# Kernel optimization log

Measured on AMD Instinct MI355X. Metric: run time of the kernel, lower is better.

## Reference

```python
import jax, jax.numpy as jnp
import numpy as np

N_NODES = 100000
IN_DIM = 128
HID = 128
N_REL = 2
N_EDGES = 500000


def setup_inputs() -> dict:
    key = jax.random.key(0)
    ks = jax.random.split(key, 12)
    x = jax.random.normal(ks[0], (N_NODES, IN_DIM), dtype=jnp.float32)
    edge_index = jax.random.randint(ks[1], (2, N_EDGES), 0, N_NODES, dtype=jnp.int64)
    edge_type = jax.random.randint(ks[2], (N_EDGES,), 0, N_REL, dtype=jnp.int64)
    def w(k, shape, fan_in):
        return jax.random.normal(k, shape, dtype=jnp.float32) / np.sqrt(fan_in)
    return {
        "x": x,
        "edge_index": edge_index,
        "edge_type": edge_type,
        "W_rel1": w(ks[3], (N_REL, IN_DIM, HID), IN_DIM),
        "W_root1": w(ks[4], (IN_DIM, HID), IN_DIM),
        "b1": jnp.zeros((HID,), jnp.float32),
        "W_rel2": w(ks[5], (N_REL, HID, HID), HID),
        "W_root2": w(ks[6], (HID, HID), HID),
        "b2": jnp.zeros((HID,), jnp.float32),
        "Wc": w(ks[7], (HID, 2), HID),
        "bc": jnp.zeros((2,), jnp.float32),
    }


def rgcn_conv(x, src, dst, edge_type, W_rel, W_root, b, n_nodes):
    """PyG RGCNConv: out_i = x_i @ W_root + b + sum_r mean_{j in N_r(i)} x_j @ W_r."""
    out = x @ W_root + b
    for r in range(W_rel.shape[0]):  # small fixed relation count
        mask = (edge_type == r).astype(x.dtype)  # [E]
        xr = x @ W_rel[r]                         # [N, dout] transform-then-gather
        msg = xr[src] * mask[:, None]             # [E, dout]
        agg = jax.ops.segment_sum(msg, dst, num_segments=n_nodes)   # [N, dout]
        cnt = jax.ops.segment_sum(mask, dst, num_segments=n_nodes)  # [N]
        out = out + agg / jnp.maximum(cnt, 1.0)[:, None]            # mean aggr
    return out


def reference(x, edge_index, edge_type, W_rel1, W_root1, b1, W_rel2, W_root2, b2, Wc, bc):
    n = x.shape[0]
    src, dst = edge_index[0], edge_index[1]
    h = rgcn_conv(x, src, dst, edge_type, W_rel1, W_root1, b1, n)
    h = jax.nn.relu(h)
    # dropout is identity at inference (training=False)
    h = rgcn_conv(h, src, dst, edge_type, W_rel2, W_root2, b2, n)
    h = jax.nn.relu(h)
    logits = h @ Wc + bc
    return logits
```

## Files before the change

### kernel.cpp

```cpp
#include <hip/hip_runtime.h>
#include <hip/hip_fp16.h>

#define N_NODES 100000
#define PAD_N   100096
#define IN_DIM 128
#define HID 128
#define N_REL 2
#define N_EDGES 500000
#define M_SEG (N_REL * N_NODES)
#define SCAN_BLK 1024
#define SCAN_NB ((M_SEG + SCAN_BLK - 1) / SCAN_BLK)

#define CVT_BLOCKS 12500
#define PACK_BLOCKS 48
#define HIST_BLOCKS 1954

#define GB_EDGES 48

typedef __attribute__((ext_vector_type(8))) _Float16 half8;
typedef __attribute__((ext_vector_type(4))) float float4v;

__device__ __forceinline__ unsigned short f2h(float f) {
    return __half_as_ushort(__float2half(f));
}

__global__ __launch_bounds__(256) void prep_kernel(
    const float* __restrict__ X, unsigned short* __restrict__ Xb,
    const float* __restrict__ Wroot1, const float* __restrict__ Wrel1,
    const float* __restrict__ Wroot2, const float* __restrict__ Wrel2,
    unsigned short* __restrict__ Wp,
    const int* __restrict__ ei, const int* __restrict__ et,
    unsigned* __restrict__ cnt)
{
    int bid = blockIdx.x;
    if (bid < CVT_BLOCKS) {
        int i = bid * 256 + threadIdx.x;
        if (i >= N_NODES * IN_DIM / 4) return;
        float4 v = ((const float4*)X)[i];
        ushort4 o;
        o.x = f2h(v.x); o.y = f2h(v.y); o.z = f2h(v.z); o.w = f2h(v.w);
        ((ushort4*)Xb)[i] = o;
    } else if (bid < CVT_BLOCKS + PACK_BLOCKS) {
        int tid = (bid - CVT_BLOCKS) * 256 + threadIdx.x;
        int layer = tid / 6144;
        int rem   = tid % 6144;
        int ks    = rem / 512;
        int rem2  = rem % 512;
        int nt    = rem2 / 64;
        int lane  = rem2 % 64;
        int seg = ks >> 2;
        int kl  = (ks & 3) * 32 + (lane >> 4) * 8;
        int chan = nt * 16 + (lane & 15);
        const float* Wroot = layer ? Wroot2 : Wroot1;
        const float* Wrel  = layer ? Wrel2  : Wrel1;
        const float* W = (seg == 0) ? Wroot : (Wrel + (size_t)(seg - 1) * 128 * 128);
        unsigned short* dst = Wp + (size_t)tid * 8;
        #pragma unroll
        for (int j = 0; j < 8; ++j)
            dst[j] = f2h(W[(size_t)(kl + j) * 128 + chan]);
    } else {
        int e = (bid - CVT_BLOCKS - PACK_BLOCKS) * 256 + threadIdx.x;
        if (e >= N_EDGES) return;
        int dst = ei[N_EDGES + e];
        int r = et[e];
        atomicAdd(cnt + (size_t)r * N_NODES + dst, 1u);
    }
}

__global__ __launch_bounds__(256) void scan1_kernel(
    const unsigned* __restrict__ cnt,
    unsigned* __restrict__ rs, unsigned* __restrict__ bsums)
{
    __shared__ unsigned sdata[256];
    int t = threadIdx.x;
    int base = blockIdx.x * SCAN_BLK + t * 4;
    unsigned v[4]; unsigned s = 0;
    #pragma unroll
    for (int j = 0; j < 4; ++j) {
        v[j] = (base + j < M_SEG) ? cnt[base + j] : 0u;
        s += v[j];
    }
    sdata[t] = s;
    __syncthreads();
    #pragma unroll
    for (int off = 1; off < 256; off <<= 1) {
        unsigned x = (t >= off) ? sdata[t - off] : 0u;
        __syncthreads();
        if (t >= off) sdata[t] += x;
        __syncthreads();
    }
    unsigned excl = (t > 0) ? sdata[t - 1] : 0u;
    if (t == 255) bsums[blockIdx.x] = sdata[255];
    unsigned run = excl;
    #pragma unroll
    for (int j = 0; j < 4; ++j) {
        if (base + j < M_SEG) rs[base + j] = run;
        run += v[j];
    }
}

__global__ __launch_bounds__(256) void scan3_kernel(
    unsigned* __restrict__ rs, const unsigned* __restrict__ bsums,
    unsigned* __restrict__ cursor)
{
    __shared__ unsigned sdata[256];
    int t = threadIdx.x;
    sdata[t] = (t < SCAN_NB) ? bsums[t] : 0u;
    __syncthreads();
    #pragma unroll
    for (int off = 1; off < 256; off <<= 1) {
        unsigned x = (t >= off) ? sdata[t - off] : 0u;
        __syncthreads();
        if (t >= off) sdata[t] += x;
        __syncthreads();
    }
    int i = blockIdx.x * blockDim.x + t;
    if (i < M_SEG) {
        int b = i >> 10;
        unsigned add = (b > 0) ? sdata[b - 1] : 0u;
        unsigned v = rs[i] + add;
        rs[i] = v;
        cursor[i] = v;
    }
    if (i == 0) rs[M_SEG] = N_EDGES;
}

__global__ __launch_bounds__(256) void fill_kernel(
    const int* __restrict__ ei, const int* __restrict__ et,
    unsigned* __restrict__ cursor, unsigned* __restrict__ csr)
{
    int e = blockIdx.x * blockDim.x + threadIdx.x;
    if (e >= N_EDGES) return;
    int src = ei[e];
    int dst = ei[N_EDGES + e];
    int r = et[e];
    unsigned pos = atomicAdd(cursor + (size_t)r * N_NODES + dst, 1u);
    csr[pos] = (unsigned)src;
}

template <bool FINAL>
__global__ __launch_bounds__(256) void gemm_kernel(
    const unsigned short* __restrict__ Xin,
    const unsigned* __restrict__ rs,
    const unsigned* __restrict__ csr,
    const unsigned short* __restrict__ Wp,
    const float* __restrict__ bias,
    unsigned short* __restrict__ Hout,
    const float* __restrict__ Wc,
    const float* __restrict__ bc,
    float* __restrict__ Out)
{
    __shared__ __align__(16) unsigned char gbuf[4][GB_EDGES * 256];

    const int t    = threadIdx.x;
    const int w    = t >> 6;
    const int lane = t & 63;
    const int l15  = lane & 15;
    const int quad = lane >> 4;
    const int rowbase = blockIdx.x * 64 + w * 16;
    const int koff = quad * 8;
    unsigned char* myBuf = &gbuf[w][0];

    const uint4* __restrict__ X4 = (const uint4*)Xin;

    __half2 a2[2][4][4];
    #pragma unroll
    for (int r = 0; r < 2; ++r)
        #pragma unroll
        for (int ksl = 0; ksl < 4; ++ksl)
            #pragma unroll
            for (int j = 0; j < 4; ++j)
                a2[r][ksl][j] = __float2half2_rn(0.f);

    const int node = rowbase + l15;
    float inv_[2] = {1.f, 1.f};

    if (rowbase < N_NODES) {
        #pragma unroll
        for (int r = 0; r < 2; ++r) {
            unsigned S = rs[(size_t)r * N_NODES + rowbase];
            unsigned E = rs[(size_t)r * N_NODES + rowbase + 16];
            unsigned st = rs[(size_t)r * N_NODES + node];
            unsigned en = rs[(size_t)r * N_NODES + node + 1];
            unsigned d = en - st;
            inv_[r] = 1.0f / (float)(d ? d : 1u);

            for (unsigned base = S; base < E; base += GB_EDGES) {
                unsigned cnt = E - base;
                if (cnt > GB_EDGES) cnt = GB_EDGES;

                unsigned ids[12];
                #pragma unroll
                for (int i = 0; i < 12; ++i) {
                    if ((unsigned)(i * 4) < cnt) {
                        unsigned e = base + (unsigned)(i * 4) + (unsigned)(lane >> 4);
                        ids[i] = csr[e < E ? e : E - 1u];
                    } else ids[i] = 0u;
                }

                #pragma unroll
                for (int i = 0; i < 12; ++i) {
                    if ((unsigned)(i * 4) < cnt) {
                        unsigned eL = (unsigned)(i * 4) + (unsigned)(lane >> 4);
                        unsigned cg = (unsigned)(lane & 15) ^ (eL & 7u);
                        const unsigned short* gp =
                            (const unsigned short*)(X4 + ((size_t)ids[i] << 4) + cg);
                        __builtin_amdgcn_global_load_lds(
                            (const __attribute__((address_space(1))) unsigned int*)gp,
                            (__attribute__((address_space(3))) unsigned int*)(myBuf + i * 1024),
                            16, 0, 0);
                    }
                }

                asm volatile("s_waitcnt vmcnt(0)" ::: "memory");
                __builtin_amdgcn_sched_barrier(0);

                unsigned lo = st > base ? st : base;
                unsigned hiB = base + cnt;
                unsigned hi = en < hiB ? en : hiB;
                for (unsigned p = lo; p < hi; ++p) {
                    unsigned eL = p - base;
                    const unsigned char* rowb = myBuf + eL * 256;
                    #pragma unroll
                    for (int ksl = 0; ksl < 4; ++ksl) {
                        unsigned pos = ((unsigned)(ksl * 4 + quad)) ^ (eL & 7u);
                        half8 h = *(const half8*)(rowb + pos * 16);
                        #pragma unroll
                        for (int j = 0; j < 4; ++j)
                            a2[r][ksl][j] = __hadd2(a2[r][ksl][j],
                                                    ((const __half2*)&h)[j]);
                    }
                }
            }
        }
    }

    half8 ag[2][4];
    #pragma unroll
    for (int r = 0; r < 2; ++r) {
        __half2 s2 = __float2half2_rn(inv_[r]);
        #pragma unroll
        for (int ksl = 0; ksl < 4; ++ksl) {
            half8 h;
            #pragma unroll
            for (int j = 0; j < 4; ++j)
                ((__half2*)&h)[j] = __hmul2(a2[r][ksl][j], s2);
            ag[r][ksl] = h;
        }
    }

    auto ldB = [&](int ks, int nt) -> half8 {
        return *(const half8*)(Wp + ((size_t)(ks * 8 + nt) * 64 + lane) * 8);
    };
    const unsigned short* aBase = Xin + (size_t)(rowbase + l15) * 128 + koff;

    float4v acc[8];
    #pragma unroll
    for (int nt = 0; nt < 8; ++nt) {
        float bv = bias[nt * 16 + l15];
        acc[nt] = float4v{bv, bv, bv, bv};
    }

    half8 ax[4];
    #pragma unroll
    for (int ksl = 0; ksl < 4; ++ksl)
        ax[ksl] = *(const half8*)(aBase + ksl * 32);

    half8 bb[3][8];
    #pragma unroll
    for (int nt = 0; nt < 8; ++nt) bb[0][nt] = ldB(0, nt);
    #pragma unroll
    for (int nt = 0; nt < 8; ++nt) bb[1][nt] = ldB(1, nt);

    #pragma unroll
    for (int ks = 0; ks < 12; ++ks) {
        if (ks + 2 < 12) {
            #pragma unroll
            for (int nt = 0; nt < 8; ++nt)
                bb[(ks + 2) % 3][nt] = ldB(ks + 2, nt);
        }
        half8 A = (ks < 4) ? ax[ks] : ag[(ks >> 2) - 1][ks & 3];
        #pragma unroll
        for (int nt = 0; nt < 8; ++nt)
            acc[nt] = __builtin_amdgcn_mfma_f32_16x16x32_f16(A, bb[ks % 3][nt], acc[nt], 0, 0, 0);
    }

    if (!FINAL) {
        #pragma unroll
        for (int rr = 0; rr < 4; ++rr) {
            int n2 = rowbase + quad * 4 + rr;
            unsigned short* hp = Hout + (size_t)n2 * 128 + l15;
            #pragma unroll
            for (int nt = 0; nt < 8; ++nt)
                hp[nt * 16] = f2h(fmaxf(acc[nt][rr], 0.f));
        }
    } else {
        float wc0[8], wc1[8];
        #pragma unroll
        for (int nt = 0; nt < 8; ++nt) {
            wc0[nt] = Wc[(nt * 16 + l15) * 2 + 0];
            wc1[nt] = Wc[(nt * 16 + l15) * 2 + 1];
        }
        float b0 = bc[0], b1 = bc[1];
        #pragma unroll
        for (int rr = 0; rr < 4; ++rr) {
            float l0 = 0.f, l1 = 0.f;
            #pragma unroll
            for (int nt = 0; nt < 8; ++nt) {
                float h = fmaxf(acc[nt][rr], 0.f);
                l0 += h * wc0[nt];
                l1 += h * wc1[nt];
            }
            #pragma unroll
            for (int off = 8; off > 0; off >>= 1) {
                l0 += __shfl_down(l0, off, 16);
                l1 += __shfl_down(l1, off, 16);
            }
            int n2 = rowbase + quad * 4 + rr;
            if (l15 == 0 && n2 < N_NODES) {
                Out[(size_t)n2 * 2 + 0] = l0 + b0;
                Out[(size_t)n2 * 2 + 1] = l1 + b1;
            }
        }
    }
}

extern "C" void kernel_launch(void* const* d_in, const int* in_sizes, int n_in,
                              void* d_out, int out_size, void* d_ws, size_t ws_size,
                              hipStream_t stream)
{
    const float* x      = (const float*)d_in[0];
    const int*   ei     = (const int*)d_in[1];
    const int*   et     = (const int*)d_in[2];
    const float* Wrel1  = (const float*)d_in[3];
    const float* Wroot1 = (const float*)d_in[4];
    const float* b1     = (const float*)d_in[5];
    const float* Wrel2  = (const float*)d_in[6];
    const float* Wroot2 = (const float*)d_in[7];
    const float* b2     = (const float*)d_in[8];
    const float* Wc     = (const float*)d_in[9];
    const float* bc     = (const float*)d_in[10];
    float* out = (float*)d_out;

    char* ws = (char*)d_ws;
    size_t off = 0;
    auto alloc = [&](size_t bytes) {
        void* p = ws + off;
        off += (bytes + 255) & ~(size_t)255;
        return p;
    };
    unsigned short* xb    = (unsigned short*)alloc((size_t)PAD_N * IN_DIM * 2);
    unsigned short* h1b   = (unsigned short*)alloc((size_t)PAD_N * HID * 2);
    unsigned short* Wp    = (unsigned short*)alloc((size_t)2 * 12 * 8 * 64 * 8 * 2);
    unsigned*       rs    = (unsigned*)alloc((size_t)(M_SEG + 1) * 4);
    unsigned*       cursor= (unsigned*)alloc((size_t)M_SEG * 4);
    unsigned*       bsums = (unsigned*)alloc(256 * 4);
    unsigned*       csr   = (unsigned*)alloc((size_t)N_EDGES * 4);

    const int edge_blocks = (N_EDGES + 255) / 256;
    const int seg_blocks  = (M_SEG + 255) / 256;
    const int gemm_blocks = PAD_N / 64;
    const int prep_blocks = CVT_BLOCKS + PACK_BLOCKS + HIST_BLOCKS;

    hipMemsetAsync(cursor, 0, (size_t)M_SEG * 4, stream);
    prep_kernel<<<prep_blocks, 256, 0, stream>>>(
        x, xb, Wroot1, Wrel1, Wroot2, Wrel2, Wp, ei, et, cursor);
    scan1_kernel<<<SCAN_NB, 256, 0, stream>>>(cursor, rs, bsums);
    scan3_kernel<<<seg_blocks, 256, 0, stream>>>(rs, bsums, cursor);
    fill_kernel<<<edge_blocks, 256, 0, stream>>>(ei, et, cursor, csr);

    gemm_kernel<false><<<gemm_blocks, 256, 0, stream>>>(
        xb, rs, csr, Wp, b1, h1b, nullptr, nullptr, nullptr);

    gemm_kernel<true><<<gemm_blocks, 256, 0, stream>>>(
        h1b, rs, csr, Wp + (size_t)12 * 8 * 64 * 8, b2, nullptr, Wc, bc, out);
}
```

Before: 285.3 us.

## Stage packed weights through LDS with async global_load_lds and vectorize hidden stores

Weight fragments for the MFMA loop are now loaded cooperatively into double-buffered LDS with global_load_lds, so four waves share each load instead of every wave reading all weights from global memory. The layer-1 weight packing permutes output channels so each lane holds eight contiguous channels, which lets the hidden activation write become one 16-byte store per row instead of scattered 2-byte stores. The X row loads are hoisted ahead of the gather phase. This adds block-wide barriers between phases and reuses the gather buffer memory as the weight staging area.

```diff
diff --git a/kernel.cpp b/kernel.cpp
--- a/kernel.cpp
+++ b/kernel.cpp
@@ -50,7 +50,7 @@
         int lane  = rem2 % 64;
         int seg = ks >> 2;
         int kl  = (ks & 3) * 32 + (lane >> 4) * 8;
-        int chan = nt * 16 + (lane & 15);
+        int chan = layer ? (nt * 16 + (lane & 15)) : ((lane & 15) * 8 + nt);
         const float* Wroot = layer ? Wroot2 : Wroot1;
         const float* Wrel  = layer ? Wrel2  : Wrel1;
         const float* W = (seg == 0) ? Wroot : (Wrel + (size_t)(seg - 1) * 128 * 128);
@@ -150,7 +150,7 @@
     const float* __restrict__ bc,
     float* __restrict__ Out)
 {
-    __shared__ __align__(16) unsigned char gbuf[4][GB_EDGES * 256];
+    __shared__ __align__(16) unsigned char lds_raw[49152];
 
     const int t    = threadIdx.x;
     const int w    = t >> 6;
@@ -159,9 +159,16 @@
     const int quad = lane >> 4;
     const int rowbase = blockIdx.x * 64 + w * 16;
     const int koff = quad * 8;
-    unsigned char* myBuf = &gbuf[w][0];
+    unsigned char* myBuf = lds_raw + w * (GB_EDGES * 256);
+    unsigned short* ldsB = (unsigned short*)lds_raw;
 
     const uint4* __restrict__ X4 = (const uint4*)Xin;
+
+    const unsigned short* aBase = Xin + (size_t)(rowbase + l15) * 128 + koff;
+    half8 ax[4];
+    #pragma unroll
+    for (int ksl = 0; ksl < 4; ++ksl)
+        ax[ksl] = *(const half8*)(aBase + ksl * 32);
 
     __half2 a2[2][4][4];
     #pragma unroll
@@ -249,50 +256,62 @@
         }
     }
 
-    auto ldB = [&](int ks, int nt) -> half8 {
-        return *(const half8*)(Wp + ((size_t)(ks * 8 + nt) * 64 + lane) * 8);
+    __syncthreads();
+
+    auto stage = [&](int ph, int buf) {
+        #pragma unroll
+        for (int fi = 0; fi < 6; ++fi) {
+            int f  = fi * 4 + w;
+            int sl = f >> 3;
+            int nt = f & 7;
+            int ks = ph * 3 + sl;
+            const unsigned short* g = Wp + ((size_t)(ks * 8 + nt) * 64 + lane) * 8;
+            unsigned short* l = ldsB + (size_t)buf * 12288 + (size_t)(sl * 8 + nt) * 512;
+            __builtin_amdgcn_global_load_lds(
+                (const __attribute__((address_space(1))) unsigned int*)g,
+                (__attribute__((address_space(3))) unsigned int*)l, 16, 0, 0);
+        }
     };
-    const unsigned short* aBase = Xin + (size_t)(rowbase + l15) * 128 + koff;
 
     float4v acc[8];
     #pragma unroll
     for (int nt = 0; nt < 8; ++nt) {
-        float bv = bias[nt * 16 + l15];
+        float bv = FINAL ? bias[nt * 16 + l15] : bias[l15 * 8 + nt];
         acc[nt] = float4v{bv, bv, bv, bv};
     }
 
-    half8 ax[4];
-    #pragma unroll
-    for (int ksl = 0; ksl < 4; ++ksl)
-        ax[ksl] = *(const half8*)(aBase + ksl * 32);
-
-    half8 bb[3][8];
-    #pragma unroll
-    for (int nt = 0; nt < 8; ++nt) bb[0][nt] = ldB(0, nt);
-    #pragma unroll
-    for (int nt = 0; nt < 8; ++nt) bb[1][nt] = ldB(1, nt);
-
-    #pragma unroll
-    for (int ks = 0; ks < 12; ++ks) {
-        if (ks + 2 < 12) {
+    stage(0, 0);
+    __syncthreads();
+
+    #pragma unroll
+    for (int ph = 0; ph < 4; ++ph) {
+        if (ph < 3) stage(ph + 1, (ph + 1) & 1);
+        #pragma unroll
+        for (int sl = 0; sl < 3; ++sl) {
+            int ks = ph * 3 + sl;
+            half8 b[8];
             #pragma unroll
             for (int nt = 0; nt < 8; ++nt)
-                bb[(ks + 2) % 3][nt] = ldB(ks + 2, nt);
-        }
-        half8 A = (ks < 4) ? ax[ks] : ag[(ks >> 2) - 1][ks & 3];
-        #pragma unroll
-        for (int nt = 0; nt < 8; ++nt)
-            acc[nt] = __builtin_amdgcn_mfma_f32_16x16x32_f16(A, bb[ks % 3][nt], acc[nt], 0, 0, 0);
+                b[nt] = *(const half8*)(ldsB + (size_t)(ph & 1) * 12288 +
+                                        (size_t)(sl * 8 + nt) * 512 + lane * 8);
+            half8 A = (ks < 4) ? ax[ks] : ag[(ks >> 2) - 1][ks & 3];
+            #pragma unroll
+            for (int nt = 0; nt < 8; ++nt)
+                acc[nt] = __builtin_amdgcn_mfma_f32_16x16x32_f16(A, b[nt], acc[nt], 0, 0, 0);
+        }
+        __syncthreads();
     }
 
     if (!FINAL) {
         #pragma unroll
         for (int rr = 0; rr < 4; ++rr) {
             int n2 = rowbase + quad * 4 + rr;
-            unsigned short* hp = Hout + (size_t)n2 * 128 + l15;
-            #pragma unroll
-            for (int nt = 0; nt < 8; ++nt)
-                hp[nt * 16] = f2h(fmaxf(acc[nt][rr], 0.f));
+            __half2 hv[4];
+            #pragma unroll
+            for (int j = 0; j < 4; ++j)
+                hv[j] = __floats2half2_rn(fmaxf(acc[2 * j][rr], 0.f),
+                                          fmaxf(acc[2 * j + 1][rr], 0.f));
+            *(uint4*)(Hout + (size_t)n2 * 128 + l15 * 8) = *(const uint4*)hv;
         }
     } else {
         float wc0[8], wc1[8];
```

After: 257.8 us. -9.6%, faster.
